# Performance work log

Measured on AMD Instinct MI355X. Metric: run time of the kernel, lower is better.

The kernel has to match this reference:

```python
import jax, jax.numpy as jnp
import numpy as np

N_S, N_C, N_L = 100000, 20000, 5000
E_U, E_T = 2000000, 500000
D_S, D_C, D_L, H = 64, 32, 128, 128
N_LAYERS = 3  # num_layers=2 -> ModuleList holds 3 hetero layers


def _sage(h_src, h_dst, src_idx, dst_idx, W_self, W_neigh, b, n_dst):
    # DGL SAGEConv 'mean': fc_self(h_dst) + fc_neigh(mean of in-neighbor src feats) + bias
    summed = jax.ops.segment_sum(h_src[src_idx], dst_idx, num_segments=n_dst)  # [n_dst, d]
    deg = jax.ops.segment_sum(jnp.ones((src_idx.shape[0],), h_src.dtype), dst_idx, num_segments=n_dst)
    h_neigh = summed / jnp.maximum(deg, 1.0)[:, None]
    return h_dst @ W_self + h_neigh @ W_neigh + b


def setup_inputs() -> dict:
    key = jax.random.key(0)
    ks = jax.random.split(key, 24)
    s = 0.05
    inp = {
        'feat_student': jax.random.normal(ks[0], (N_S, D_S), jnp.float32),
        'feat_concept': jax.random.normal(ks[1], (N_C, D_C), jnp.float32),
        'feat_lecture': jax.random.normal(ks[2], (N_L, D_L), jnp.float32),
        'W_fs': jax.random.normal(ks[3], (D_S, H), jnp.float32) * s,
        'b_fs': jnp.zeros((H,), jnp.float32),
        'W_fc': jax.random.normal(ks[4], (D_C, H), jnp.float32) * s,
        'b_fc': jnp.zeros((H,), jnp.float32),
        'W_fl': jax.random.normal(ks[5], (D_L, H), jnp.float32) * s,
        'b_fl': jnp.zeros((H,), jnp.float32),
        # per-layer, per-relation SAGE params (all dims 128 so they stack)
        'W_self_u': jax.random.normal(ks[6], (N_LAYERS, H, H), jnp.float32) * s,
        'W_neigh_u': jax.random.normal(ks[7], (N_LAYERS, H, H), jnp.float32) * s,
        'b_u': jnp.zeros((N_LAYERS, H), jnp.float32),
        'W_self_t': jax.random.normal(ks[8], (N_LAYERS, H, H), jnp.float32) * s,
        'W_neigh_t': jax.random.normal(ks[9], (N_LAYERS, H, H), jnp.float32) * s,
        'b_t': jnp.zeros((N_LAYERS, H), jnp.float32),
        'und_src': jax.random.randint(ks[10], (E_U,), 0, N_S, jnp.int32),
        'und_dst': jax.random.randint(ks[11], (E_U,), 0, N_C, jnp.int32),
        'tea_src': jax.random.randint(ks[12], (E_T,), 0, N_L, jnp.int32),
        'tea_dst': jax.random.randint(ks[13], (E_T,), 0, N_C, jnp.int32),
    }
    return inp


def reference(feat_student, feat_concept, feat_lecture,
              W_fs, b_fs, W_fc, b_fc, W_fl, b_fl,
              W_self_u, W_neigh_u, b_u, W_self_t, W_neigh_t, b_t,
              und_src, und_dst, tea_src, tea_dst):
    # input projections per node type
    h_s = feat_student @ W_fs + b_fs
    h_c = feat_concept @ W_fc + b_fc
    h_l = feat_lecture @ W_fl + b_fl
    n_c = h_c.shape[0]
    for i in range(N_LAYERS):
        ou = _sage(h_s, h_c, und_src, und_dst, W_self_u[i], W_neigh_u[i], b_u[i], n_c)
        ot = _sage(h_l, h_c, tea_src, tea_dst, W_self_t[i], W_neigh_t[i], b_t[i], n_c)
        # HeteroGraphConv cross-relation aggregate: 'mean' on layer 0, default 'sum' after
        h_c = (ou + ot) * (0.5 if i == 0 else 1.0)
        if i != N_LAYERS - 1:
            h_c = jax.nn.relu(h_c)  # dropout is identity in eval mode
        # student/lecture are never destination types -> features pass through
    return h_c  # [N_C, 128] concept embeddings
```

## Files before the change

### kernel.cpp

```cpp
#include <hip/hip_runtime.h>
#include <hip/hip_bf16.h>
#include <cstdint>
#include <cstddef>

#define NS_ 100000
#define NC_ 20000
#define NL_ 5000
#define EU_ 2000000
#define ET_ 500000
#define H_  128

#define NBK_ 625
#define CHK_ 3907
#define UBLK_ 512
#define TBLK_ 128
#define CAPU_ 3600
#define CAPT_ 1024
#define SEDGE_ 3712

typedef __attribute__((ext_vector_type(8))) short bs8;
typedef __attribute__((ext_vector_type(4))) float f32x4;
typedef __attribute__((ext_vector_type(2))) float v2f;

__device__ inline short bf_rne(float f) {
    unsigned u = __float_as_uint(f);
    u = (u + 0x7fffu + ((u >> 16) & 1u)) >> 16;
    return (short)u;
}
__device__ inline unsigned pack_bf16x2(float a, float b) {
    return ((unsigned)(unsigned short)bf_rne(a)) |
           (((unsigned)(unsigned short)bf_rne(b)) << 16);
}
__device__ inline float bflo(unsigned w) { return __uint_as_float(w << 16); }
__device__ inline float bfhi(unsigned w) { return __uint_as_float(w & 0xffff0000u); }

#define B_SCU UBLK_
#define B_SCT TBLK_
#define B_CVT 512
#define B_PACK 480
#define B_BC 2
#define B_PROJ 313
#define B_TOTAL (B_SCU + B_SCT + B_CVT + B_PACK + B_BC + B_PROJ)

__global__ __launch_bounds__(256) void prep_fused_kernel(
    const int* __restrict__ und_dst, const int* __restrict__ und_src,
    const int* __restrict__ tea_dst, const int* __restrict__ tea_src,
    unsigned* __restrict__ gcurU, unsigned* __restrict__ gcurT,
    unsigned* __restrict__ binnedU, unsigned* __restrict__ binnedT,
    const float* __restrict__ feat_s, unsigned* __restrict__ fs8,
    const float* __restrict__ feat_l, unsigned* __restrict__ flb,
    const float* __restrict__ Wsu, const float* __restrict__ Wnu,
    const float* __restrict__ Wst, const float* __restrict__ Wnt,
    const float* __restrict__ W_fs, const float* __restrict__ W_fl,
    short* __restrict__ WpL,
    const float* __restrict__ bu, const float* __restrict__ bt,
    const float* __restrict__ b_fs, const float* __restrict__ b_fl,
    float* __restrict__ bc,
    const float* __restrict__ feat_c, const float* __restrict__ W_fc,
    const float* __restrict__ b_fc, short* __restrict__ hc2A)
{
    __shared__ unsigned smem[5760];
    const int b = blockIdx.x;
    const int tid = threadIdx.x;

    if (b < B_SCU + B_SCT) {
        const bool isU = (b < B_SCU);
        const int blk = isU ? b : (b - B_SCU);
        const int nEdge = isU ? EU_ : ET_;
        const int* dstp = isU ? und_dst : tea_dst;
        const int* srcp = isU ? und_src : tea_src;
        unsigned* gcur = isU ? gcurU : gcurT;
        unsigned* binned = isU ? binnedU : binnedT;
        const unsigned cap = isU ? CAPU_ : CAPT_;
        unsigned* sed = smem;
        unsigned* cnt = smem + 3968;
        unsigned* pre = smem + 4736;
        unsigned* par = smem + 5504;
        for (int i = tid; i < 768; i += 256) cnt[i] = 0;
        __syncthreads();
        const int start = blk * CHK_;
        const int end = min(start + CHK_, nEdge);
        for (int i = start + tid; i < end; i += 256)
            atomicAdd(&cnt[dstp[i] >> 5], 1u);
        __syncthreads();
        unsigned c0 = cnt[3 * tid], c1 = cnt[3 * tid + 1], c2 = cnt[3 * tid + 2];
        unsigned s = c0 + c1 + c2;
        par[tid] = s;
        __syncthreads();
        unsigned sum = s;
        for (int d = 1; d < 256; d <<= 1) {
            unsigned x = (tid >= d) ? par[tid - d] : 0;
            __syncthreads();
            sum += x;
            par[tid] = sum;
            __syncthreads();
        }
        unsigned p = sum - s;
        pre[3 * tid] = p;
        pre[3 * tid + 1] = p + c0;
        pre[3 * tid + 2] = p + c0 + c1;
        __syncthreads();
        for (int k = tid; k < NBK_; k += 256) {
            unsigned L = cnt[k];
            unsigned W = L ? atomicAdd(&gcur[k], L) : 0;
            if (W + L > cap) W = cap - L;
            cnt[k] = k * cap + W - pre[k];
        }
        __syncthreads();
        for (int i = start + tid; i < end; i += 256) {
            int d = dstp[i];
            unsigned k = (unsigned)d >> 5;
            unsigned e = (unsigned)srcp[i] | ((unsigned)(d & 31) << 17) | (k << 22);
            unsigned pos = atomicAdd(&pre[k], 1u);
            sed[pos] = e;
        }
        __syncthreads();
        const int n = end - start;
        for (int i = tid; i < n; i += 256) {
            unsigned e = sed[i];
            binned[cnt[e >> 22] + i] = e & 0x3FFFFFu;
        }
    } else if (b < B_SCU + B_SCT + B_CVT) {
        int i = (b - B_SCU - B_SCT) * 256 + tid;
        const int stride = B_CVT * 256;
        const int nS = NS_ * 16;
        const int nTot = nS + NL_ * 64;
        for (; i < nTot; i += stride) {
            if (i < nS) {
                const float4 v = ((const float4*)feat_s)[i];
                unsigned r = __builtin_amdgcn_cvt_pk_fp8_f32(v.x, v.y, 0, false);
                r = __builtin_amdgcn_cvt_pk_fp8_f32(v.z, v.w, r, true);
                fs8[i] = r;
            } else {
                int j = i - nS;
                float2 v = ((const float2*)feat_l)[j];
                flb[j] = pack_bf16x2(v.x, v.y);
            }
        }
    } else if (b < B_SCU + B_SCT + B_CVT + B_PACK) {
        int i = (b - B_SCU - B_SCT - B_CVT) * 256 + tid;
        int j = i & 7;
        int lane = (i >> 3) & 63;
        int nt = (i >> 9) & 7;
        int ktAll = i >> 12;
        int l = ktAll / 10;
        int kt = ktAll - l * 10;
        int k = kt * 32 + (lane >> 4) * 8 + j;
        int n = nt * 16 + (lane & 15);
        const size_t WL = (size_t)l * H_ * H_;
        float v;
        if (k < 128) {
            v = Wsu[WL + k * H_ + n] + Wst[WL + k * H_ + n];
        } else if (k < 192) {
            int a = k - 128;
            v = 0.f;
            for (int t = 0; t < 128; t++) v += W_fs[a * H_ + t] * Wnu[WL + t * H_ + n];
        } else {
            int a = k - 192;
            v = 0.f;
            for (int t = 0; t < 128; t++) v += W_fl[a * H_ + t] * Wnt[WL + t * H_ + n];
        }
        WpL[i] = bf_rne(v);
    } else if (b < B_SCU + B_SCT + B_CVT + B_PACK + B_BC) {
        int i = (b - B_SCU - B_SCT - B_CVT - B_PACK) * 256 + tid;
        if (i < 3 * H_) {
            int l = i >> 7, c = i & 127;
            const size_t WL = (size_t)l * H_ * H_;
            float v = bu[i] + bt[i];
            for (int j2 = 0; j2 < 128; j2++)
                v += b_fs[j2] * Wnu[WL + j2 * H_ + c] + b_fl[j2] * Wnt[WL + j2 * H_ + c];
            bc[i] = v;
        }
    } else {
        short* lw = (short*)smem;
        const int bp = b - (B_SCU + B_SCT + B_CVT + B_PACK + B_BC);
        for (int idx = tid; idx < 4096; idx += 256) {
            int j = idx & 7;
            int lane = (idx >> 3) & 63;
            int nt = idx >> 9;
            int k = (lane >> 4) * 8 + j;
            int n = nt * 16 + (lane & 15);
            lw[idx] = bf_rne(W_fc[k * H_ + n]);
        }
        __syncthreads();
        const int lane = tid & 63;
        const int wv = tid >> 6;
        const int row0 = bp * 64 + wv * 16;
        const int q = lane >> 4;
        const int rA = min(row0 + (lane & 15), NC_ - 1);
        f32x4 acc[8];
#pragma unroll
        for (int i = 0; i < 8; i++) acc[i] = (f32x4){0.f, 0.f, 0.f, 0.f};
        const float* xp = feat_c + (size_t)rA * 32 + q * 8;
        float4 xa = *(const float4*)xp;
        float4 xb = *(const float4*)(xp + 4);
        bs8 af;
        af[0] = bf_rne(xa.x); af[1] = bf_rne(xa.y); af[2] = bf_rne(xa.z); af[3] = bf_rne(xa.w);
        af[4] = bf_rne(xb.x); af[5] = bf_rne(xb.y); af[6] = bf_rne(xb.z); af[7] = bf_rne(xb.w);
#pragma unroll
        for (int nt = 0; nt < 8; nt++) {
            bs8 bfr = *(const bs8*)(lw + (nt * 64 + lane) * 8);
            acc[nt] = __builtin_amdgcn_mfma_f32_16x16x32_bf16(af, bfr, acc[nt], 0, 0, 0);
        }
        const int colb = lane & 15;
#pragma unroll
        for (int nt = 0; nt < 8; nt++) {
            int col = nt * 16 + colb;
            float bv = b_fc[col];
#pragma unroll
            for (int r = 0; r < 4; r++) {
                int row = row0 + q * 4 + r;
                if (row < NC_) hc2A[(size_t)row * H_ + col] = bf_rne(acc[nt][r] + bv);
            }
        }
    }
}

__global__ __launch_bounds__(256) void agg_kernel(
    const unsigned* __restrict__ gcurU, const unsigned* __restrict__ binnedU,
    const uint2* __restrict__ fs8, unsigned* __restrict__ aggFu,
    const unsigned* __restrict__ gcurT, const unsigned* __restrict__ binnedT,
    const uint4* __restrict__ flb4, unsigned* __restrict__ aggFt)
{
    __shared__ unsigned sedge[SEDGE_];
    __shared__ unsigned sh[32], soff[33], scur[32];
    const int b = blockIdx.x;
    const int tid = threadIdx.x;
    const bool isU = (b < NBK_);
    const int bb = isU ? b : (b - NBK_);
    const unsigned* binned = isU ? binnedU : binnedT;
    const unsigned cap = isU ? CAPU_ : CAPT_;
    const size_t start = (size_t)bb * cap;
    const int n = min((int)(isU ? gcurU : gcurT)[bb], (int)cap);

    if (tid < 32) sh[tid] = 0;
    __syncthreads();
    for (int i = tid; i < n; i += 256)
        atomicAdd(&sh[(binned[start + i] >> 17) & 31], 1u);
    __syncthreads();
    if (tid == 0) {
        unsigned r = 0;
        for (int j = 0; j < 32; j++) {
            unsigned v = sh[j];
            soff[j] = r;
            scur[j] = r;
            r += v;
        }
        soff[32] = r;
    }
    __syncthreads();
    for (int i = tid; i < n; i += 256) {
        unsigned p = binned[start + i];
        unsigned pos = atomicAdd(&scur[(p >> 17) & 31], 1u);
        if (pos < SEDGE_) sedge[pos] = p & 0x1FFFFu;
    }
    __syncthreads();

    const int g = tid >> 3;
    const int sub = tid & 7;
    const int gs = (int)soff[g];
    const int ge = (int)min(soff[g + 1], (unsigned)SEDGE_);
    const int c = bb * 32 + g;
    const float inv = 1.f / (float)max(ge - gs, 1);

    if (isU) {
        float a[8];
#pragma unroll
        for (int i = 0; i < 8; i++) a[i] = 0.f;
        int e = gs;
        for (; e + 2 <= ge; e += 2) {
            unsigned s0 = sedge[e], s1 = sedge[e + 1];
            uint2 w0 = fs8[(size_t)s0 * 8 + sub];
            uint2 w1 = fs8[(size_t)s1 * 8 + sub];
            v2f p0 = __builtin_amdgcn_cvt_pk_f32_fp8(w0.x, false);
            v2f p1 = __builtin_amdgcn_cvt_pk_f32_fp8(w0.x, true);
            v2f p2 = __builtin_amdgcn_cvt_pk_f32_fp8(w0.y, false);
            v2f p3 = __builtin_amdgcn_cvt_pk_f32_fp8(w0.y, true);
            a[0] += p0.x; a[1] += p0.y; a[2] += p1.x; a[3] += p1.y;
            a[4] += p2.x; a[5] += p2.y; a[6] += p3.x; a[7] += p3.y;
            p0 = __builtin_amdgcn_cvt_pk_f32_fp8(w1.x, false);
            p1 = __builtin_amdgcn_cvt_pk_f32_fp8(w1.x, true);
            p2 = __builtin_amdgcn_cvt_pk_f32_fp8(w1.y, false);
            p3 = __builtin_amdgcn_cvt_pk_f32_fp8(w1.y, true);
            a[0] += p0.x; a[1] += p0.y; a[2] += p1.x; a[3] += p1.y;
            a[4] += p2.x; a[5] += p2.y; a[6] += p3.x; a[7] += p3.y;
        }
        if (e < ge) {
            uint2 w0 = fs8[(size_t)sedge[e] * 8 + sub];
            v2f p0 = __builtin_amdgcn_cvt_pk_f32_fp8(w0.x, false);
            v2f p1 = __builtin_amdgcn_cvt_pk_f32_fp8(w0.x, true);
            v2f p2 = __builtin_amdgcn_cvt_pk_f32_fp8(w0.y, false);
            v2f p3 = __builtin_amdgcn_cvt_pk_f32_fp8(w0.y, true);
            a[0] += p0.x; a[1] += p0.y; a[2] += p1.x; a[3] += p1.y;
            a[4] += p2.x; a[5] += p2.y; a[6] += p3.x; a[7] += p3.y;
        }
        uint4 o;
        o.x = pack_bf16x2(a[0] * inv, a[1] * inv);
        o.y = pack_bf16x2(a[2] * inv, a[3] * inv);
        o.z = pack_bf16x2(a[4] * inv, a[5] * inv);
        o.w = pack_bf16x2(a[6] * inv, a[7] * inv);
        ((uint4*)aggFu)[(size_t)c * 8 + sub] = o;
    } else {
        float a[16];
#pragma unroll
        for (int i = 0; i < 16; i++) a[i] = 0.f;
        for (int e = gs; e < ge; e++) {
            unsigned src = sedge[e];
            uint4 w0 = flb4[(size_t)src * 16 + sub * 2];
            uint4 w1 = flb4[(size_t)src * 16 + sub * 2 + 1];
            a[0] += bflo(w0.x); a[1] += bfhi(w0.x);
            a[2] += bflo(w0.y); a[3] += bfhi(w0.y);
            a[4] += bflo(w0.z); a[5] += bfhi(w0.z);
            a[6] += bflo(w0.w); a[7] += bfhi(w0.w);
            a[8]  += bflo(w1.x); a[9]  += bfhi(w1.x);
            a[10] += bflo(w1.y); a[11] += bfhi(w1.y);
            a[12] += bflo(w1.z); a[13] += bfhi(w1.z);
            a[14] += bflo(w1.w); a[15] += bfhi(w1.w);
        }
        uint4 o0, o1;
        o0.x = pack_bf16x2(a[0] * inv, a[1] * inv);
        o0.y = pack_bf16x2(a[2] * inv, a[3] * inv);
        o0.z = pack_bf16x2(a[4] * inv, a[5] * inv);
        o0.w = pack_bf16x2(a[6] * inv, a[7] * inv);
        o1.x = pack_bf16x2(a[8] * inv, a[9] * inv);
        o1.y = pack_bf16x2(a[10] * inv, a[11] * inv);
        o1.z = pack_bf16x2(a[12] * inv, a[13] * inv);
        o1.w = pack_bf16x2(a[14] * inv, a[15] * inv);
        ((uint4*)aggFt)[(size_t)c * 16 + sub * 2] = o0;
        ((uint4*)aggFt)[(size_t)c * 16 + sub * 2 + 1] = o1;
    }
}

template <bool FINAL>
__global__ __launch_bounds__(256) void layer_mfma(
    const unsigned* __restrict__ A0, const unsigned* __restrict__ A1,
    const unsigned* __restrict__ A2, const short* __restrict__ Wp,
    const float* __restrict__ bias, float scale,
    short* __restrict__ out_bf, float* __restrict__ out_f32, int n)
{
    const int lane = threadIdx.x & 63;
    const int wv = threadIdx.x >> 6;
    const int row0 = blockIdx.x * 64 + wv * 16;
    const int q = lane >> 4;
    const int rA = min(row0 + (lane & 15), n - 1);
    f32x4 acc[8];
#pragma unroll
    for (int i = 0; i < 8; i++) acc[i] = (f32x4){0.f, 0.f, 0.f, 0.f};
#pragma unroll
    for (int kt = 0; kt < 10; kt++) {
        const unsigned* A;
        int rowU, off;
        if (kt < 4)      { A = A0; rowU = 64; off = kt * 16; }
        else if (kt < 6) { A = A1; rowU = 32; off = (kt - 4) * 16; }
        else             { A = A2; rowU = 64; off = (kt - 6) * 16; }
        bs8 af = *(const bs8*)(A + (size_t)rA * rowU + off + q * 4);
        const short* wp = Wp + (size_t)kt * 8 * 512;
#pragma unroll
        for (int nt = 0; nt < 8; nt++) {
            bs8 bfr = *(const bs8*)(wp + ((size_t)nt * 64 + lane) * 8);
            acc[nt] = __builtin_amdgcn_mfma_f32_16x16x32_bf16(af, bfr, acc[nt], 0, 0, 0);
        }
    }
    const int colb = lane & 15;
#pragma unroll
    for (int nt = 0; nt < 8; nt++) {
        int col = nt * 16 + colb;
        float bv = bias[col];
#pragma unroll
        for (int r = 0; r < 4; r++) {
            int row = row0 + q * 4 + r;
            if (row < n) {
                float v = (acc[nt][r] + bv) * scale;
                if constexpr (!FINAL) {
                    v = fmaxf(v, 0.f);
                    out_bf[(size_t)row * H_ + col] = bf_rne(v);
                } else {
                    out_f32[(size_t)row * H_ + col] = v;
                }
            }
        }
    }
}

extern "C" void kernel_launch(void* const* d_in, const int* in_sizes, int n_in,
                              void* d_out, int out_size, void* d_ws, size_t ws_size,
                              hipStream_t stream)
{
    (void)in_sizes; (void)n_in; (void)out_size; (void)ws_size;
    const float* feat_s = (const float*)d_in[0];
    const float* feat_c = (const float*)d_in[1];
    const float* feat_l = (const float*)d_in[2];
    const float* W_fs = (const float*)d_in[3];
    const float* b_fs = (const float*)d_in[4];
    const float* W_fc = (const float*)d_in[5];
    const float* b_fc = (const float*)d_in[6];
    const float* W_fl = (const float*)d_in[7];
    const float* b_fl = (const float*)d_in[8];
    const float* W_self_u  = (const float*)d_in[9];
    const float* W_neigh_u = (const float*)d_in[10];
    const float* b_u = (const float*)d_in[11];
    const float* W_self_t  = (const float*)d_in[12];
    const float* W_neigh_t = (const float*)d_in[13];
    const float* b_t = (const float*)d_in[14];
    const int* und_src = (const int*)d_in[15];
    const int* und_dst = (const int*)d_in[16];
    const int* tea_src = (const int*)d_in[17];
    const int* tea_dst = (const int*)d_in[18];
    float* out = (float*)d_out;

    char* ws = (char*)d_ws;
    size_t o = 0;
    auto alloc = [&](size_t bytes) -> char* {
        char* p = ws + o;
        o += (bytes + 255) & ~(size_t)255;
        return p;
    };
    unsigned* fs8  = (unsigned*)alloc((size_t)NS_ * 16 * 4);
    unsigned* flb  = (unsigned*)alloc((size_t)NL_ * 64 * 4);
    short* hc2A = (short*)alloc((size_t)NC_ * H_ * 2);
    short* hc2B = (short*)alloc((size_t)NC_ * H_ * 2);
    unsigned* aggFu = (unsigned*)alloc((size_t)NC_ * 32 * 4);
    unsigned* aggFt = (unsigned*)alloc((size_t)NC_ * 64 * 4);
    short* WpL = (short*)alloc((size_t)3 * 10 * 8 * 64 * 8 * 2);
    float* bc  = (float*)alloc((size_t)3 * H_ * 4);
    unsigned* gcurU = (unsigned*)alloc((size_t)NBK_ * 4);
    unsigned* gcurT = (unsigned*)alloc((size_t)NBK_ * 4);
    unsigned* binnedU = (unsigned*)alloc((size_t)NBK_ * CAPU_ * 4);
    unsigned* binnedT = (unsigned*)alloc((size_t)NBK_ * CAPT_ * 4);

    hipMemsetAsync(gcurU, 0, (size_t)((char*)binnedU - (char*)gcurU), stream);

    prep_fused_kernel<<<B_TOTAL, 256, 0, stream>>>(
        und_dst, und_src, tea_dst, tea_src, gcurU, gcurT, binnedU, binnedT,
        feat_s, fs8, feat_l, flb,
        W_self_u, W_neigh_u, W_self_t, W_neigh_t, W_fs, W_fl, WpL,
        b_u, b_t, b_fs, b_fl, bc,
        feat_c, W_fc, b_fc, hc2A);

    agg_kernel<<<2 * NBK_, 256, 0, stream>>>(
        gcurU, binnedU, (const uint2*)fs8, aggFu,
        gcurT, binnedT, (const uint4*)flb, aggFt);

    layer_mfma<false><<<(NC_ + 63) / 64, 256, 0, stream>>>(
        (const unsigned*)hc2A, aggFu, aggFt, WpL, bc, 0.5f, hc2B, nullptr, NC_);
    layer_mfma<false><<<(NC_ + 63) / 64, 256, 0, stream>>>(
        (const unsigned*)hc2B, aggFu, aggFt, WpL + 40960, bc + H_, 1.0f, hc2A, nullptr, NC_);
    layer_mfma<true><<<(NC_ + 63) / 64, 256, 0, stream>>>(
        (const unsigned*)hc2A, aggFu, aggFt, WpL + 2 * 40960, bc + 2 * H_, 1.0f,
        nullptr, out, NC_);
}
```

Measured before the change: 237.4 us.

## Fuse concept projection and three SAGE layers into one MFMA kernel

Replaces the three per-layer layer_mfma launches with a single kernel in which each wave keeps its 16 concept rows resident. The concept projection, now moved out of the prep kernel, and each layer's hidden state pass between stages through a per-wave LDS tile instead of global memory. The aggregated neighbour fragments are loaded once and reused across all three layers. This removes two kernel launches and the global round trips of the hidden-state buffers, at the cost of more registers and LDS per block and a serial chain of work per wave.

```diff
diff --git a/kernel.cpp b/kernel.cpp
--- a/kernel.cpp
+++ b/kernel.cpp
@@ -39,8 +39,8 @@
 #define B_CVT 512
 #define B_PACK 480
 #define B_BC 2
-#define B_PROJ 313
-#define B_TOTAL (B_SCU + B_SCT + B_CVT + B_PACK + B_BC + B_PROJ)
+#define B_WFC 16
+#define B_TOTAL (B_SCU + B_SCT + B_CVT + B_PACK + B_BC + B_WFC)
 
 __global__ __launch_bounds__(256) void prep_fused_kernel(
     const int* __restrict__ und_dst, const int* __restrict__ und_src,
@@ -56,8 +56,7 @@
     const float* __restrict__ bu, const float* __restrict__ bt,
     const float* __restrict__ b_fs, const float* __restrict__ b_fl,
     float* __restrict__ bc,
-    const float* __restrict__ feat_c, const float* __restrict__ W_fc,
-    const float* __restrict__ b_fc, short* __restrict__ hc2A)
+    const float* __restrict__ W_fc, short* __restrict__ WpC)
 {
     __shared__ unsigned smem[5760];
     const int b = blockIdx.x;
@@ -172,47 +171,13 @@
             bc[i] = v;
         }
     } else {
-        short* lw = (short*)smem;
-        const int bp = b - (B_SCU + B_SCT + B_CVT + B_PACK + B_BC);
-        for (int idx = tid; idx < 4096; idx += 256) {
-            int j = idx & 7;
-            int lane = (idx >> 3) & 63;
-            int nt = idx >> 9;
-            int k = (lane >> 4) * 8 + j;
-            int n = nt * 16 + (lane & 15);
-            lw[idx] = bf_rne(W_fc[k * H_ + n]);
-        }
-        __syncthreads();
-        const int lane = tid & 63;
-        const int wv = tid >> 6;
-        const int row0 = bp * 64 + wv * 16;
-        const int q = lane >> 4;
-        const int rA = min(row0 + (lane & 15), NC_ - 1);
-        f32x4 acc[8];
-#pragma unroll
-        for (int i = 0; i < 8; i++) acc[i] = (f32x4){0.f, 0.f, 0.f, 0.f};
-        const float* xp = feat_c + (size_t)rA * 32 + q * 8;
-        float4 xa = *(const float4*)xp;
-        float4 xb = *(const float4*)(xp + 4);
-        bs8 af;
-        af[0] = bf_rne(xa.x); af[1] = bf_rne(xa.y); af[2] = bf_rne(xa.z); af[3] = bf_rne(xa.w);
-        af[4] = bf_rne(xb.x); af[5] = bf_rne(xb.y); af[6] = bf_rne(xb.z); af[7] = bf_rne(xb.w);
-#pragma unroll
-        for (int nt = 0; nt < 8; nt++) {
-            bs8 bfr = *(const bs8*)(lw + (nt * 64 + lane) * 8);
-            acc[nt] = __builtin_amdgcn_mfma_f32_16x16x32_bf16(af, bfr, acc[nt], 0, 0, 0);
-        }
-        const int colb = lane & 15;
-#pragma unroll
-        for (int nt = 0; nt < 8; nt++) {
-            int col = nt * 16 + colb;
-            float bv = b_fc[col];
-#pragma unroll
-            for (int r = 0; r < 4; r++) {
-                int row = row0 + q * 4 + r;
-                if (row < NC_) hc2A[(size_t)row * H_ + col] = bf_rne(acc[nt][r] + bv);
-            }
-        }
+        int i = (b - (B_SCU + B_SCT + B_CVT + B_PACK + B_BC)) * 256 + tid;
+        int j = i & 7;
+        int lane = (i >> 3) & 63;
+        int nt = (i >> 9) & 7;
+        int k = (lane >> 4) * 8 + j;
+        int n = nt * 16 + (lane & 15);
+        WpC[i] = bf_rne(W_fc[k * H_ + n]);
     }
 }
 
@@ -331,51 +296,99 @@
     }
 }
 
-template <bool FINAL>
-__global__ __launch_bounds__(256) void layer_mfma(
-    const unsigned* __restrict__ A0, const unsigned* __restrict__ A1,
-    const unsigned* __restrict__ A2, const short* __restrict__ Wp,
-    const float* __restrict__ bias, float scale,
-    short* __restrict__ out_bf, float* __restrict__ out_f32, int n)
+__global__ __launch_bounds__(256) void layers_fused_kernel(
+    const float* __restrict__ feat_c, const short* __restrict__ WpC,
+    const float* __restrict__ b_fc,
+    const unsigned* __restrict__ aggFu, const unsigned* __restrict__ aggFt,
+    const short* __restrict__ WpL, const float* __restrict__ bc,
+    float* __restrict__ out)
 {
-    const int lane = threadIdx.x & 63;
-    const int wv = threadIdx.x >> 6;
+    __shared__ short lds[4][16 * 132];
+    const int tid = threadIdx.x;
+    const int lane = tid & 63;
+    const int wv = tid >> 6;
     const int row0 = blockIdx.x * 64 + wv * 16;
     const int q = lane >> 4;
-    const int rA = min(row0 + (lane & 15), n - 1);
+    const int m = lane & 15;
+    const int rA = min(row0 + m, NC_ - 1);
+    short* tile = lds[wv];
+
+    bs8 fuF[2], ftF[4], hcF[4];
+#pragma unroll
+    for (int kt = 0; kt < 2; kt++)
+        fuF[kt] = *(const bs8*)(aggFu + (size_t)rA * 32 + kt * 16 + q * 4);
+#pragma unroll
+    for (int kt = 0; kt < 4; kt++)
+        ftF[kt] = *(const bs8*)(aggFt + (size_t)rA * 64 + kt * 16 + q * 4);
+
     f32x4 acc[8];
 #pragma unroll
     for (int i = 0; i < 8; i++) acc[i] = (f32x4){0.f, 0.f, 0.f, 0.f};
-#pragma unroll
-    for (int kt = 0; kt < 10; kt++) {
-        const unsigned* A;
-        int rowU, off;
-        if (kt < 4)      { A = A0; rowU = 64; off = kt * 16; }
-        else if (kt < 6) { A = A1; rowU = 32; off = (kt - 4) * 16; }
-        else             { A = A2; rowU = 64; off = (kt - 6) * 16; }
-        bs8 af = *(const bs8*)(A + (size_t)rA * rowU + off + q * 4);
-        const short* wp = Wp + (size_t)kt * 8 * 512;
+    {
+        const float* xp = feat_c + (size_t)rA * 32 + q * 8;
+        float4 xa = *(const float4*)xp;
+        float4 xb = *(const float4*)(xp + 4);
+        bs8 af;
+        af[0] = bf_rne(xa.x); af[1] = bf_rne(xa.y); af[2] = bf_rne(xa.z); af[3] = bf_rne(xa.w);
+        af[4] = bf_rne(xb.x); af[5] = bf_rne(xb.y); af[6] = bf_rne(xb.z); af[7] = bf_rne(xb.w);
 #pragma unroll
         for (int nt = 0; nt < 8; nt++) {
-            bs8 bfr = *(const bs8*)(wp + ((size_t)nt * 64 + lane) * 8);
+            bs8 bfr = *(const bs8*)(WpC + ((size_t)nt * 64 + lane) * 8);
             acc[nt] = __builtin_amdgcn_mfma_f32_16x16x32_bf16(af, bfr, acc[nt], 0, 0, 0);
         }
     }
-    const int colb = lane & 15;
 #pragma unroll
     for (int nt = 0; nt < 8; nt++) {
-        int col = nt * 16 + colb;
-        float bv = bias[col];
-#pragma unroll
-        for (int r = 0; r < 4; r++) {
-            int row = row0 + q * 4 + r;
-            if (row < n) {
-                float v = (acc[nt][r] + bv) * scale;
-                if constexpr (!FINAL) {
-                    v = fmaxf(v, 0.f);
-                    out_bf[(size_t)row * H_ + col] = bf_rne(v);
-                } else {
-                    out_f32[(size_t)row * H_ + col] = v;
+        int col = nt * 16 + m;
+        float bv = b_fc[col];
+#pragma unroll
+        for (int r = 0; r < 4; r++)
+            tile[(q * 4 + r) * 132 + col] = bf_rne(acc[nt][r] + bv);
+    }
+#pragma unroll
+    for (int kt = 0; kt < 4; kt++)
+        hcF[kt] = *(const bs8*)(tile + m * 132 + kt * 32 + q * 8);
+
+#pragma unroll
+    for (int l = 0; l < 3; l++) {
+#pragma unroll
+        for (int i = 0; i < 8; i++) acc[i] = (f32x4){0.f, 0.f, 0.f, 0.f};
+        const short* wl = WpL + (size_t)l * 40960;
+#pragma unroll
+        for (int kt = 0; kt < 10; kt++) {
+            bs8 af = (kt < 4) ? hcF[kt] : ((kt < 6) ? fuF[kt - 4] : ftF[kt - 6]);
+            const short* wp = wl + (size_t)kt * 4096;
+#pragma unroll
+            for (int nt = 0; nt < 8; nt++) {
+                bs8 bfr = *(const bs8*)(wp + ((size_t)nt * 64 + lane) * 8);
+                acc[nt] = __builtin_amdgcn_mfma_f32_16x16x32_bf16(af, bfr, acc[nt], 0, 0, 0);
+            }
+        }
+        const float scale = (l == 0) ? 0.5f : 1.0f;
+        const float* bl = bc + l * H_;
+        if (l < 2) {
+#pragma unroll
+            for (int nt = 0; nt < 8; nt++) {
+                int col = nt * 16 + m;
+                float bv = bl[col];
+#pragma unroll
+                for (int r = 0; r < 4; r++)
+                    tile[(q * 4 + r) * 132 + col] =
+                        bf_rne(fmaxf((acc[nt][r] + bv) * scale, 0.f));
+            }
+#pragma unroll
+            for (int kt = 0; kt < 4; kt++)
+                hcF[kt] = *(const bs8*)(tile + m * 132 + kt * 32 + q * 8);
+        } else {
+#pragma unroll
+            for (int nt = 0; nt < 8; nt++) {
+                int col = nt * 16 + m;
+                float bv = bl[col];
+#pragma unroll
+                for (int r = 0; r < 4; r++) {
+                    int row = row0 + q * 4 + r;
+                    if (row < NC_)
+                        out[(size_t)row * H_ + col] = (acc[nt][r] + bv) * scale;
                 }
             }
         }
@@ -417,11 +430,10 @@
     };
     unsigned* fs8  = (unsigned*)alloc((size_t)NS_ * 16 * 4);
     unsigned* flb  = (unsigned*)alloc((size_t)NL_ * 64 * 4);
-    short* hc2A = (short*)alloc((size_t)NC_ * H_ * 2);
-    short* hc2B = (short*)alloc((size_t)NC_ * H_ * 2);
     unsigned* aggFu = (unsigned*)alloc((size_t)NC_ * 32 * 4);
     unsigned* aggFt = (unsigned*)alloc((size_t)NC_ * 64 * 4);
     short* WpL = (short*)alloc((size_t)3 * 10 * 8 * 64 * 8 * 2);
+    short* WpC = (short*)alloc((size_t)8 * 64 * 8 * 2);
     float* bc  = (float*)alloc((size_t)3 * H_ * 4);
     unsigned* gcurU = (unsigned*)alloc((size_t)NBK_ * 4);
     unsigned* gcurT = (unsigned*)alloc((size_t)NBK_ * 4);
@@ -435,17 +447,12 @@
         feat_s, fs8, feat_l, flb,
         W_self_u, W_neigh_u, W_self_t, W_neigh_t, W_fs, W_fl, WpL,
         b_u, b_t, b_fs, b_fl, bc,
-        feat_c, W_fc, b_fc, hc2A);
+        W_fc, WpC);
 
     agg_kernel<<<2 * NBK_, 256, 0, stream>>>(
         gcurU, binnedU, (const uint2*)fs8, aggFu,
         gcurT, binnedT, (const uint4*)flb, aggFt);
 
-    layer_mfma<false><<<(NC_ + 63) / 64, 256, 0, stream>>>(
-        (const unsigned*)hc2A, aggFu, aggFt, WpL, bc, 0.5f, hc2B, nullptr, NC_);
-    layer_mfma<false><<<(NC_ + 63) / 64, 256, 0, stream>>>(
-        (const unsigned*)hc2B, aggFu, aggFt, WpL + 40960, bc + H_, 1.0f, hc2A, nullptr, NC_);
-    layer_mfma<true><<<(NC_ + 63) / 64, 256, 0, stream>>>(
-        (const unsigned*)hc2A, aggFu, aggFt, WpL + 2 * 40960, bc + 2 * H_, 1.0f,
-        nullptr, out, NC_);
-}
+    layers_fused_kernel<<<(NC_ + 63) / 64, 256, 0, stream>>>(
+        feat_c, WpC, b_fc, aggFu, aggFt, WpL, bc, out);
+}
```

New measurement: 215.7 us. 1.1x faster.
